# Performance work log

Hardware: AMD Instinct MI355X
Metric: run time of the kernel (lower is better)

## Reference

```python
import jax, jax.numpy as jnp
import numpy as np

N_NODES = 100000
IN_DIM = 64
HID = 128
HID2 = HID // 2
N_CLASSES = 2
N_EDGES = 1600000
BN_EPS = 1e-5


def setup_inputs() -> dict:
    key = jax.random.key(0)
    ks = jax.random.split(key, 12)
    x = jax.random.normal(ks[0], (N_NODES, IN_DIM), dtype=jnp.float32)
    edge_index = jax.random.randint(ks[1], (2, N_EDGES), 0, N_NODES, dtype=jnp.int64)
    s = lambda k, shp, fan: jax.random.normal(k, shp, dtype=jnp.float32) / np.sqrt(fan)
    return {
        "x": x,
        "edge_index": edge_index,
        # SAGEConv1: lin_l (on aggregated neighbors, has bias), lin_r (root, no bias)
        "W1_l": s(ks[2], (IN_DIM, HID), IN_DIM),
        "b1_l": jnp.zeros((HID,), jnp.float32),
        "W1_r": s(ks[3], (IN_DIM, HID), IN_DIM),
        # SAGEConv2
        "W2_l": s(ks[4], (HID, HID2), HID),
        "b2_l": jnp.zeros((HID2,), jnp.float32),
        "W2_r": s(ks[5], (HID, HID2), HID),
        # BatchNorm (eval mode: running stats)
        "bn1_gamma": jnp.ones((HID,), jnp.float32),
        "bn1_beta": jnp.zeros((HID,), jnp.float32),
        "bn1_mean": jax.random.normal(ks[6], (HID,), dtype=jnp.float32) * 0.1,
        "bn1_var": jax.random.uniform(ks[7], (HID,), minval=0.5, maxval=1.5, dtype=jnp.float32),
        "bn2_gamma": jnp.ones((HID2,), jnp.float32),
        "bn2_beta": jnp.zeros((HID2,), jnp.float32),
        "bn2_mean": jax.random.normal(ks[8], (HID2,), dtype=jnp.float32) * 0.1,
        "bn2_var": jax.random.uniform(ks[9], (HID2,), minval=0.5, maxval=1.5, dtype=jnp.float32),
        # classifier
        "Wc": s(ks[10], (HID2, N_CLASSES), HID2),
        "bc": jnp.zeros((N_CLASSES,), jnp.float32),
    }


def _sage_mean(h, src, dst, Wl, bl, Wr, n_nodes):
    # gather source-node features along edges, scatter-mean into destinations
    msg = h[src]                                            # [E, D]
    summed = jax.ops.segment_sum(msg, dst, num_segments=n_nodes)  # [N, D]
    cnt = jax.ops.segment_sum(jnp.ones_like(dst, dtype=h.dtype), dst, num_segments=n_nodes)
    mean = summed / jnp.maximum(cnt, 1.0)[:, None]
    return mean @ Wl + bl + h @ Wr


def _bn_eval(h, gamma, beta, mean, var):
    return (h - mean) * (gamma * jax.lax.rsqrt(var + BN_EPS)) + beta


def reference(x, edge_index, W1_l, b1_l, W1_r, W2_l, b2_l, W2_r,
              bn1_gamma, bn1_beta, bn1_mean, bn1_var,
              bn2_gamma, bn2_beta, bn2_mean, bn2_var, Wc, bc):
    src, dst = edge_index[0], edge_index[1]
    n = x.shape[0]
    h = _sage_mean(x, src, dst, W1_l, b1_l, W1_r, n)
    h = jax.nn.relu(_bn_eval(h, bn1_gamma, bn1_beta, bn1_mean, bn1_var))
    h = _sage_mean(h, src, dst, W2_l, b2_l, W2_r, n)
    h = jax.nn.relu(_bn_eval(h, bn2_gamma, bn2_beta, bn2_mean, bn2_var))
    return h @ Wc + bc  # logits [N, num_classes]
```

## Files before the change

kernel.cpp:

```cpp
#include <hip/hip_runtime.h>
#include <math.h>

#define N_NODES 100000
#define IN_DIM 64
#define HID 128
#define HID2 64
#define N_EDGES 1600000
#define BN_EPS 1e-5f

#define NPB 128
#define NB 782
#define BIN_BLOCKS 391
#define BIN_CHUNK 4096
#define SORT_CAP 4096
#define CAST_BLOCKS 6250

typedef __attribute__((ext_vector_type(8))) __bf16 bf16x8;
typedef __attribute__((ext_vector_type(4))) float f32x4;
typedef __attribute__((ext_vector_type(2))) float f32x2;
typedef __attribute__((ext_vector_type(8))) unsigned short u16x8;

__device__ __forceinline__ unsigned short f2bf(float f) {
    unsigned int u = __builtin_bit_cast(unsigned int, f);
    u += 0x7fffu + ((u >> 16) & 1u);
    return (unsigned short)(u >> 16);
}

__device__ __forceinline__ void accum_fp8x8(float a[8], uint2 v) {
    f32x2 p0 = __builtin_amdgcn_cvt_pk_f32_fp8((int)v.x, false);
    f32x2 p1 = __builtin_amdgcn_cvt_pk_f32_fp8((int)v.x, true);
    f32x2 p2 = __builtin_amdgcn_cvt_pk_f32_fp8((int)v.y, false);
    f32x2 p3 = __builtin_amdgcn_cvt_pk_f32_fp8((int)v.y, true);
    a[0] += p0.x; a[1] += p0.y; a[2] += p1.x; a[3] += p1.y;
    a[4] += p2.x; a[5] += p2.y; a[6] += p3.x; a[7] += p3.y;
}

__global__ __launch_bounds__(256) void prep_all(
    const float* __restrict__ x,
    const float* __restrict__ W1l, const float* __restrict__ W1r,
    const float* __restrict__ W2l, const float* __restrict__ W2r,
    unsigned short* __restrict__ Wf1, unsigned short* __restrict__ Wf2,
    unsigned short* __restrict__ Abuf,
    unsigned char* __restrict__ x8,
    int* __restrict__ bucketTotal)
{
    const int bid = blockIdx.x;
    if (bid < 16) {
        int task = bid * 4 + (threadIdx.x >> 6);
        int lane = threadIdx.x & 63;
        int m  = task >> 5;
        int nt = (task >> 2) & 7;
        int kt = task & 3;
        int col = nt * 16 + (lane & 15);
        int k0  = kt * 32 + (lane >> 4) * 8;
        unsigned short tmp[8];
        #pragma unroll
        for (int e = 0; e < 8; ++e) {
            int k = k0 + e;
            float v;
            if (m == 0) v = (k < 64) ? W1l[k * HID + col] : W1r[(k - 64) * HID + col];
            else        v = (col < 64) ? W2l[k * HID2 + col] : W2r[k * HID2 + (col - 64)];
            tmp[e] = f2bf(v);
        }
        unsigned short* dst = ((m == 0) ? Wf1 : Wf2)
                            + ((size_t)((nt * 4 + kt) * 64 + lane)) * 8;
        *(u16x8*)dst = *(const u16x8*)tmp;
    } else if (bid < 16 + CAST_BLOCKS) {
        int tid = (bid - 16) * 256 + threadIdx.x;
        int node = tid >> 4;
        int q    = tid & 15;
        float4 v = ((const float4*)x)[tid];
        unsigned short o[4] = {f2bf(v.x), f2bf(v.y), f2bf(v.z), f2bf(v.w)};
        *(uint2*)(Abuf + (size_t)node * 128 + 64 + q * 4) = *(const uint2*)o;
        int p = __builtin_amdgcn_cvt_pk_fp8_f32(v.x, v.y, 0, false);
        p     = __builtin_amdgcn_cvt_pk_fp8_f32(v.z, v.w, p, true);
        *(unsigned int*)(x8 + (size_t)node * 64 + q * 4) = (unsigned int)p;
    } else {
        for (int i = threadIdx.x; i < NB; i += 256) bucketTotal[i] = 0;
    }
}

__global__ __launch_bounds__(256) void bin_count(
    const int* __restrict__ dst,
    int* __restrict__ bucketTotal,
    int* __restrict__ perBlockBase)
{
    __shared__ int cnt[NB];
    const int t = threadIdx.x;
    for (int i = t; i < NB; i += 256) cnt[i] = 0;
    __syncthreads();
    const int e40 = blockIdx.x * (BIN_CHUNK / 4);
    const int4* dst4 = (const int4*)dst;
    #pragma unroll
    for (int i = 0; i < BIN_CHUNK / 4 / 256; ++i) {
        int ei = e40 + i * 256 + t;
        if (ei < N_EDGES / 4) {
            int4 d = dst4[ei];
            atomicAdd(&cnt[d.x >> 7], 1);
            atomicAdd(&cnt[d.y >> 7], 1);
            atomicAdd(&cnt[d.z >> 7], 1);
            atomicAdd(&cnt[d.w >> 7], 1);
        }
    }
    __syncthreads();
    for (int b = t; b < NB; b += 256) {
        int c = cnt[b];
        if (c) perBlockBase[blockIdx.x * NB + b] = atomicAdd(&bucketTotal[b], c);
    }
}

__global__ __launch_bounds__(1024) void bucket_scan(
    const int* __restrict__ bucketTotal, int* __restrict__ bucketStart)
{
    __shared__ int s[1024];
    const int t = threadIdx.x;
    int v = (t < NB) ? bucketTotal[t] : 0;
    s[t] = v;
    __syncthreads();
    #pragma unroll
    for (int off = 1; off < 1024; off <<= 1) {
        int u = (t >= off) ? s[t - off] : 0;
        __syncthreads();
        s[t] += u;
        __syncthreads();
    }
    if (t < NB) bucketStart[t] = s[t] - v;
    if (t == 0) bucketStart[NB] = N_EDGES;
}

__global__ __launch_bounds__(256) void bin_write(
    const int* __restrict__ src, const int* __restrict__ dst,
    const int* __restrict__ bucketStart,
    const int* __restrict__ perBlockBase,
    unsigned int* __restrict__ binned)
{
    __shared__ int cur[NB];
    const int t = threadIdx.x;
    for (int i = t; i < NB; i += 256) cur[i] = 0;
    __syncthreads();
    const int e40 = blockIdx.x * (BIN_CHUNK / 4);
    const int4* dst4 = (const int4*)dst;
    const int4* src4 = (const int4*)src;
    #pragma unroll
    for (int i = 0; i < BIN_CHUNK / 4 / 256; ++i) {
        int ei = e40 + i * 256 + t;
        if (ei < N_EDGES / 4) {
            int4 d = dst4[ei];
            int4 s = src4[ei];
            int ds[4] = {d.x, d.y, d.z, d.w};
            int ss[4] = {s.x, s.y, s.z, s.w};
            #pragma unroll
            for (int k = 0; k < 4; ++k) {
                int b = ds[k] >> 7;
                int pos = bucketStart[b] + perBlockBase[blockIdx.x * NB + b]
                        + atomicAdd(&cur[b], 1);
                binned[pos] = ((unsigned int)ss[k] << 7) | (unsigned int)(ds[k] & 127);
            }
        }
    }
}

__global__ __launch_bounds__(256) void bucket_sort(
    const unsigned int* __restrict__ binned,
    const int* __restrict__ bucketStart,
    int* __restrict__ sortedSrc,
    int* __restrict__ rowStart)
{
    __shared__ unsigned int stage[SORT_CAP];
    __shared__ int hist[NPB];
    __shared__ int cur[NPB];

    const int b  = blockIdx.x;
    const int t  = threadIdx.x;
    const int bs = bucketStart[b];
    const int be = bucketStart[b + 1];
    const int total = be - bs;

    if (t < NPB) hist[t] = 0;
    __syncthreads();

    if (total <= SORT_CAP) {
        for (int i = t; i < total; i += 256) {
            unsigned int p = binned[bs + i];
            stage[i] = p;
            atomicAdd(&hist[p & 127], 1);
        }
        __syncthreads();
        int orig = (t < NPB) ? hist[t] : 0;
        __syncthreads();
        #pragma unroll
        for (int off = 1; off < NPB; off <<= 1) {
            int v = (t < NPB && t >= off) ? hist[t - off] : 0;
            __syncthreads();
            if (t < NPB) hist[t] += v;
            __syncthreads();
        }
        if (t < NPB) {
            int excl = hist[t] - orig;
            int node = b * NPB + t;
            if (node < N_NODES) rowStart[node] = bs + excl;
            cur[t] = excl;
        }
        if (b == 0 && t == 0) rowStart[N_NODES] = N_EDGES;
        __syncthreads();
        for (int i = t; i < total; i += 256) {
            unsigned int p = stage[i];
            int pos = atomicAdd(&cur[p & 127], 1);
            sortedSrc[bs + pos] = (int)(p >> 7);
        }
    } else {
        for (int i = t; i < total; i += 256)
            atomicAdd(&hist[binned[bs + i] & 127], 1);
        __syncthreads();
        int orig = (t < NPB) ? hist[t] : 0;
        __syncthreads();
        #pragma unroll
        for (int off = 1; off < NPB; off <<= 1) {
            int v = (t < NPB && t >= off) ? hist[t - off] : 0;
            __syncthreads();
            if (t < NPB) hist[t] += v;
            __syncthreads();
        }
        if (t < NPB) {
            int excl = hist[t] - orig;
            int node = b * NPB + t;
            if (node < N_NODES) rowStart[node] = bs + excl;
            cur[t] = excl;
        }
        if (b == 0 && t == 0) rowStart[N_NODES] = N_EDGES;
        __syncthreads();
        for (int i = t; i < total; i += 256) {
            unsigned int p = binned[bs + i];
            int pos = atomicAdd(&cur[p & 127], 1);
            sortedSrc[bs + pos] = (int)(p >> 7);
        }
    }
}

__global__ __launch_bounds__(256) void gather1_e(
    const int* __restrict__ rowStart,
    const int* __restrict__ sortedSrc,
    const unsigned char* __restrict__ x8,
    unsigned short* __restrict__ Abuf)
{
    const int node = (int)((blockIdx.x * 256u + threadIdx.x) >> 3);
    const int lane = threadIdx.x & 63;
    const int f    = lane & 7;
    const int nb   = lane & 56;
    const int b = rowStart[node], e = rowStart[node + 1];

    float a0[8] = {}, a1[8] = {}, a2[8] = {}, a3[8] = {};

    for (int base = b; base < e; base += 8) {
        const int cnt = min(e - base, 8);
        int srcv = (base + f < e) ? sortedSrc[base + f] : 0;
        int i = 0;
        for (; i + 4 <= cnt; i += 4) {
            int s0 = __shfl(srcv, nb + i);
            int s1 = __shfl(srcv, nb + i + 1);
            int s2 = __shfl(srcv, nb + i + 2);
            int s3 = __shfl(srcv, nb + i + 3);
            accum_fp8x8(a0, *(const uint2*)(x8 + (size_t)s0 * 64 + f * 8));
            accum_fp8x8(a1, *(const uint2*)(x8 + (size_t)s1 * 64 + f * 8));
            accum_fp8x8(a2, *(const uint2*)(x8 + (size_t)s2 * 64 + f * 8));
            accum_fp8x8(a3, *(const uint2*)(x8 + (size_t)s3 * 64 + f * 8));
        }
        for (; i < cnt; ++i) {
            int s0 = __shfl(srcv, nb + i);
            accum_fp8x8(a0, *(const uint2*)(x8 + (size_t)s0 * 64 + f * 8));
        }
    }
    #pragma unroll
    for (int i = 0; i < 8; ++i) a0[i] = (a0[i] + a1[i]) + (a2[i] + a3[i]);

    float inv = 1.0f / fmaxf((float)(e - b), 1.0f);
    unsigned short o[8];
    #pragma unroll
    for (int i = 0; i < 8; ++i) o[i] = f2bf(a0[i] * inv);
    *(uint4*)(Abuf + (size_t)node * 128 + f * 8) = *(const uint4*)o;
}

__global__ __launch_bounds__(256, 4) void gemm_fused_mfma(
    const unsigned short* __restrict__ Abuf,
    const unsigned short* __restrict__ Wf1,
    const unsigned short* __restrict__ Wf2,
    const float* __restrict__ b1l,
    const float* __restrict__ g1, const float* __restrict__ be1,
    const float* __restrict__ m1, const float* __restrict__ v1,
    const float* __restrict__ b2l,
    unsigned char* __restrict__ t1f8,
    unsigned short* __restrict__ r1bf)
{
    __shared__ unsigned short Al[64 * 136];

    const int t = threadIdx.x;
    const int w = t >> 6, l = t & 63;
    const int n0 = blockIdx.x * 64;

    {
        const int node = t >> 2, q = t & 3;
        const int nn = n0 + node;
        const uint4* srcp = (const uint4*)(Abuf + (size_t)nn * 128) + q * 4;
        uint4 z; z.x = z.y = z.z = z.w = 0u;
        unsigned short* drow = &Al[node * 136 + q * 32];
        #pragma unroll
        for (int i = 0; i < 4; ++i) {
            uint4 v = (nn < N_NODES) ? srcp[i] : z;
            *(uint4*)(drow + i * 8) = v;
        }
    }
    __syncthreads();

    const int row = l & 15, kq = l >> 4;

    f32x4 acc[4][2];
    #pragma unroll
    for (int a = 0; a < 4; ++a)
        #pragma unroll
        for (int b = 0; b < 2; ++b) acc[a][b] = (f32x4)(0.0f);

    #pragma unroll
    for (int kt = 0; kt < 4; ++kt) {
        bf16x8 bfr[2];
        #pragma unroll
        for (int n = 0; n < 2; ++n)
            bfr[n] = __builtin_bit_cast(bf16x8,
                *(const u16x8*)(Wf1 + ((size_t)(((2 * w + n) * 4 + kt) * 64 + l)) * 8));
        #pragma unroll
        for (int mt = 0; mt < 4; ++mt) {
            bf16x8 afr = __builtin_bit_cast(bf16x8,
                *(const u16x8*)&Al[(mt * 16 + row) * 136 + kt * 32 + kq * 8]);
            #pragma unroll
            for (int n = 0; n < 2; ++n)
                acc[mt][n] = __builtin_amdgcn_mfma_f32_16x16x32_bf16(
                    afr, bfr[n], acc[mt][n], 0, 0, 0);
        }
    }
    __syncthreads();

    #pragma unroll
    for (int n = 0; n < 2; ++n) {
        int j = w * 32 + n * 16 + (l & 15);
        float s  = g1[j] * rsqrtf(v1[j] + BN_EPS);
        float of = be1[j] + (b1l[j] - m1[j]) * s;
        #pragma unroll
        for (int mt = 0; mt < 4; ++mt) {
            #pragma unroll
            for (int i = 0; i < 4; ++i) {
                float h = fmaxf(fmaf(acc[mt][n][i], s, of), 0.0f);
                Al[(mt * 16 + kq * 4 + i) * 136 + j] = f2bf(h);
            }
        }
    }
    __syncthreads();

    f32x4 acc2[4][2];
    #pragma unroll
    for (int a = 0; a < 4; ++a)
        #pragma unroll
        for (int b = 0; b < 2; ++b) acc2[a][b] = (f32x4)(0.0f);

    #pragma unroll
    for (int kt = 0; kt < 4; ++kt) {
        bf16x8 bfr[2];
        #pragma unroll
        for (int n = 0; n < 2; ++n)
            bfr[n] = __builtin_bit_cast(bf16x8,
                *(const u16x8*)(Wf2 + ((size_t)(((2 * w + n) * 4 + kt) * 64 + l)) * 8));
        #pragma unroll
        for (int mt = 0; mt < 4; ++mt) {
            bf16x8 afr = __builtin_bit_cast(bf16x8,
                *(const u16x8*)&Al[(mt * 16 + row) * 136 + kt * 32 + kq * 8]);
            #pragma unroll
            for (int n = 0; n < 2; ++n)
                acc2[mt][n] = __builtin_amdgcn_mfma_f32_16x16x32_bf16(
                    afr, bfr[n], acc2[mt][n], 0, 0, 0);
        }
    }

    #pragma unroll
    for (int n = 0; n < 2; ++n) {
        int j = w * 32 + n * 16 + (l & 15);
        float bl = (w >= 2) ? b2l[j - 64] : 0.0f;
        #pragma unroll
        for (int mt = 0; mt < 4; ++mt) {
            #pragma unroll
            for (int i = 0; i < 4; ++i) {
                int node = n0 + mt * 16 + kq * 4 + i;
                if (node < N_NODES) {
                    float vv = acc2[mt][n][i];
                    if (w < 2) {
                        int p = __builtin_amdgcn_cvt_pk_fp8_f32(vv, vv, 0, false);
                        t1f8[(size_t)node * 64 + j] = (unsigned char)(p & 0xff);
                    } else {
                        r1bf[(size_t)node * 64 + (j - 64)] = f2bf(vv + bl);
                    }
                }
            }
        }
    }
}

__global__ __launch_bounds__(256) void gather2_e(
    const unsigned char* __restrict__ t1f8,
    const int* __restrict__ rowStart,
    const int* __restrict__ sortedSrc,
    const unsigned short* __restrict__ r1bf,
    const float* __restrict__ g2, const float* __restrict__ be2,
    const float* __restrict__ m2, const float* __restrict__ v2,
    const float* __restrict__ Wc, const float* __restrict__ bc,
    float* __restrict__ out)
{
    const int node = (int)((blockIdx.x * 256u + threadIdx.x) >> 3);
    const int lane = threadIdx.x & 63;
    const int f    = lane & 7;
    const int nb   = lane & 56;
    const int b = rowStart[node], e = rowStart[node + 1];

    float a0[8] = {}, a1[8] = {}, a2[8] = {}, a3[8] = {};

    for (int base = b; base < e; base += 8) {
        const int cnt = min(e - base, 8);
        int srcv = (base + f < e) ? sortedSrc[base + f] : 0;
        int i = 0;
        for (; i + 4 <= cnt; i += 4) {
            int s0 = __shfl(srcv, nb + i);
            int s1 = __shfl(srcv, nb + i + 1);
            int s2 = __shfl(srcv, nb + i + 2);
            int s3 = __shfl(srcv, nb + i + 3);
            accum_fp8x8(a0, *(const uint2*)(t1f8 + (size_t)s0 * 64 + f * 8));
            accum_fp8x8(a1, *(const uint2*)(t1f8 + (size_t)s1 * 64 + f * 8));
            accum_fp8x8(a2, *(const uint2*)(t1f8 + (size_t)s2 * 64 + f * 8));
            accum_fp8x8(a3, *(const uint2*)(t1f8 + (size_t)s3 * 64 + f * 8));
        }
        for (; i < cnt; ++i) {
            int s0 = __shfl(srcv, nb + i);
            accum_fp8x8(a0, *(const uint2*)(t1f8 + (size_t)s0 * 64 + f * 8));
        }
    }
    #pragma unroll
    for (int i = 0; i < 8; ++i) a0[i] = (a0[i] + a1[i]) + (a2[i] + a3[i]);

    const float inv = 1.0f / fmaxf((float)(e - b), 1.0f);
    const int f0 = f * 8;
    uint4 rv = *(const uint4*)(r1bf + (size_t)node * 64 + f0);
    unsigned int rw[4] = {rv.x, rv.y, rv.z, rv.w};
    float l0 = 0.f, l1 = 0.f;
    #pragma unroll
    for (int i = 0; i < 8; ++i) {
        int fe = f0 + i;
        unsigned int w = rw[i >> 1];
        float rr = (i & 1) ? __builtin_bit_cast(float, w)
                           : __builtin_bit_cast(float, w << 16);
        float pre = a0[i] * inv + rr;
        float s   = g2[fe] * rsqrtf(v2[fe] + BN_EPS);
        float h2  = fmaxf((pre - m2[fe]) * s + be2[fe], 0.0f);
        l0 = fmaf(h2, Wc[fe * 2 + 0], l0);
        l1 = fmaf(h2, Wc[fe * 2 + 1], l1);
    }
    #pragma unroll
    for (int off = 4; off > 0; off >>= 1) {
        l0 += __shfl_xor(l0, off);
        l1 += __shfl_xor(l1, off);
    }
    if (f == 0) {
        out[(size_t)node * 2 + 0] = l0 + bc[0];
        out[(size_t)node * 2 + 1] = l1 + bc[1];
    }
}

extern "C" void kernel_launch(void* const* d_in, const int* in_sizes, int n_in,
                              void* d_out, int out_size, void* d_ws, size_t ws_size,
                              hipStream_t stream)
{
    const float* x    = (const float*)d_in[0];
    const int*   eidx = (const int*)d_in[1];
    const float* W1l  = (const float*)d_in[2];
    const float* b1l  = (const float*)d_in[3];
    const float* W1r  = (const float*)d_in[4];
    const float* W2l  = (const float*)d_in[5];
    const float* b2l  = (const float*)d_in[6];
    const float* W2r  = (const float*)d_in[7];
    const float* g1   = (const float*)d_in[8];
    const float* be1  = (const float*)d_in[9];
    const float* m1   = (const float*)d_in[10];
    const float* v1   = (const float*)d_in[11];
    const float* g2   = (const float*)d_in[12];
    const float* be2  = (const float*)d_in[13];
    const float* m2   = (const float*)d_in[14];
    const float* v2   = (const float*)d_in[15];
    const float* Wc   = (const float*)d_in[16];
    const float* bc   = (const float*)d_in[17];
    float* out = (float*)d_out;

    const int* src = eidx;
    const int* dst = eidx + N_EDGES;

    char* ws = (char*)d_ws;
    size_t off = 0;
    auto alloc = [&](size_t bytes) { void* p = ws + off; off = (off + bytes + 255) & ~(size_t)255; return p; };
    int* bucketTotal  = (int*)alloc((size_t)NB * 4);
    int* bucketStart  = (int*)alloc((size_t)(NB + 1) * 4);
    int* perBlockBase = (int*)alloc((size_t)BIN_BLOCKS * NB * 4);
    unsigned int* binned = (unsigned int*)alloc((size_t)N_EDGES * 4);
    int* sortedSrc    = (int*)alloc((size_t)N_EDGES * 4);
    int* rowStart     = (int*)alloc((size_t)(N_NODES + 1) * 4);
    unsigned short* Wf1  = (unsigned short*)alloc(128 * 128 * 2);
    unsigned short* Wf2  = (unsigned short*)alloc(128 * 128 * 2);
    unsigned short* Abuf = (unsigned short*)alloc((size_t)N_NODES * 128 * 2);
    unsigned char*  x8   = (unsigned char*)alloc((size_t)N_NODES * 64);
    unsigned char*  t1f8 = (unsigned char*)alloc((size_t)N_NODES * 64);
    unsigned short* r1bf = (unsigned short*)alloc((size_t)N_NODES * 64 * 2);

    const int gemmGrid    = (N_NODES + 63) / 64;
    const int gatherGrid  = (N_NODES * 8) / 256;

    prep_all<<<16 + CAST_BLOCKS + 1, 256, 0, stream>>>(
        x, W1l, W1r, W2l, W2r, Wf1, Wf2, Abuf, x8, bucketTotal);

    bin_count  <<<BIN_BLOCKS, 256, 0, stream>>>(dst, bucketTotal, perBlockBase);
    bucket_scan<<<1, 1024, 0, stream>>>(bucketTotal, bucketStart);
    bin_write  <<<BIN_BLOCKS, 256, 0, stream>>>(src, dst, bucketStart, perBlockBase, binned);
    bucket_sort<<<NB, 256, 0, stream>>>(binned, bucketStart, sortedSrc, rowStart);

    gather1_e<<<gatherGrid, 256, 0, stream>>>(rowStart, sortedSrc, x8, Abuf);

    gemm_fused_mfma<<<gemmGrid, 256, 0, stream>>>(
        Abuf, Wf1, Wf2, b1l, g1, be1, m1, v1, b2l, t1f8, r1bf);

    gather2_e<<<gatherGrid, 256, 0, stream>>>(
        t1f8, rowStart, sortedSrc, r1bf, g2, be2, m2, v2, Wc, bc, out);
}
```

Before: 139.9 us.

## Fuse layer-1 neighbor gather into the MFMA GEMM kernel via shared memory

Removes the separate gather1 kernel and performs the fp8 neighbor mean aggregation inside the GEMM block, writing results directly into the shared-memory A tile. The Abuf round trip through global memory and one kernel launch are eliminated, and x is now stored as a compact 64-wide bf16 buffer. Each node uses 4 threads loading 16 bytes per edge instead of 8 threads loading 8 bytes. The trade-off is that the GEMM block now carries the irregular gather latency, with fewer threads per node and less memory-level parallelism per node.

```diff
diff --git a/kernel.cpp b/kernel.cpp
--- a/kernel.cpp
+++ b/kernel.cpp
@@ -35,12 +35,23 @@
     a[4] += p2.x; a[5] += p2.y; a[6] += p3.x; a[7] += p3.y;
 }
 
+__device__ __forceinline__ void accum_fp8x16(float a[16], uint4 v) {
+    unsigned int w[4] = {v.x, v.y, v.z, v.w};
+    #pragma unroll
+    for (int k = 0; k < 4; ++k) {
+        f32x2 lo = __builtin_amdgcn_cvt_pk_f32_fp8((int)w[k], false);
+        f32x2 hi = __builtin_amdgcn_cvt_pk_f32_fp8((int)w[k], true);
+        a[4*k+0] += lo.x; a[4*k+1] += lo.y;
+        a[4*k+2] += hi.x; a[4*k+3] += hi.y;
+    }
+}
+
 __global__ __launch_bounds__(256) void prep_all(
     const float* __restrict__ x,
     const float* __restrict__ W1l, const float* __restrict__ W1r,
     const float* __restrict__ W2l, const float* __restrict__ W2r,
     unsigned short* __restrict__ Wf1, unsigned short* __restrict__ Wf2,
-    unsigned short* __restrict__ Abuf,
+    unsigned short* __restrict__ xbf,
     unsigned char* __restrict__ x8,
     int* __restrict__ bucketTotal)
 {
@@ -71,7 +82,7 @@
         int q    = tid & 15;
         float4 v = ((const float4*)x)[tid];
         unsigned short o[4] = {f2bf(v.x), f2bf(v.y), f2bf(v.z), f2bf(v.w)};
-        *(uint2*)(Abuf + (size_t)node * 128 + 64 + q * 4) = *(const uint2*)o;
+        *(uint2*)(xbf + (size_t)node * 64 + q * 4) = *(const uint2*)o;
         int p = __builtin_amdgcn_cvt_pk_fp8_f32(v.x, v.y, 0, false);
         p     = __builtin_amdgcn_cvt_pk_fp8_f32(v.z, v.w, p, true);
         *(unsigned int*)(x8 + (size_t)node * 64 + q * 4) = (unsigned int)p;
@@ -237,51 +248,11 @@
     }
 }
 
-__global__ __launch_bounds__(256) void gather1_e(
+__global__ __launch_bounds__(256, 4) void gemm_fused_g(
     const int* __restrict__ rowStart,
     const int* __restrict__ sortedSrc,
     const unsigned char* __restrict__ x8,
-    unsigned short* __restrict__ Abuf)
-{
-    const int node = (int)((blockIdx.x * 256u + threadIdx.x) >> 3);
-    const int lane = threadIdx.x & 63;
-    const int f    = lane & 7;
-    const int nb   = lane & 56;
-    const int b = rowStart[node], e = rowStart[node + 1];
-
-    float a0[8] = {}, a1[8] = {}, a2[8] = {}, a3[8] = {};
-
-    for (int base = b; base < e; base += 8) {
-        const int cnt = min(e - base, 8);
-        int srcv = (base + f < e) ? sortedSrc[base + f] : 0;
-        int i = 0;
-        for (; i + 4 <= cnt; i += 4) {
-            int s0 = __shfl(srcv, nb + i);
-            int s1 = __shfl(srcv, nb + i + 1);
-            int s2 = __shfl(srcv, nb + i + 2);
-            int s3 = __shfl(srcv, nb + i + 3);
-            accum_fp8x8(a0, *(const uint2*)(x8 + (size_t)s0 * 64 + f * 8));
-            accum_fp8x8(a1, *(const uint2*)(x8 + (size_t)s1 * 64 + f * 8));
-            accum_fp8x8(a2, *(const uint2*)(x8 + (size_t)s2 * 64 + f * 8));
-            accum_fp8x8(a3, *(const uint2*)(x8 + (size_t)s3 * 64 + f * 8));
-        }
-        for (; i < cnt; ++i) {
-            int s0 = __shfl(srcv, nb + i);
-            accum_fp8x8(a0, *(const uint2*)(x8 + (size_t)s0 * 64 + f * 8));
-        }
-    }
-    #pragma unroll
-    for (int i = 0; i < 8; ++i) a0[i] = (a0[i] + a1[i]) + (a2[i] + a3[i]);
-
-    float inv = 1.0f / fmaxf((float)(e - b), 1.0f);
-    unsigned short o[8];
-    #pragma unroll
-    for (int i = 0; i < 8; ++i) o[i] = f2bf(a0[i] * inv);
-    *(uint4*)(Abuf + (size_t)node * 128 + f * 8) = *(const uint4*)o;
-}
-
-__global__ __launch_bounds__(256, 4) void gemm_fused_mfma(
-    const unsigned short* __restrict__ Abuf,
+    const unsigned short* __restrict__ xbf,
     const unsigned short* __restrict__ Wf1,
     const unsigned short* __restrict__ Wf2,
     const float* __restrict__ b1l,
@@ -296,17 +267,64 @@
     const int t = threadIdx.x;
     const int w = t >> 6, l = t & 63;
     const int n0 = blockIdx.x * 64;
+    const int r   = t >> 2;
+    const int sub = t & 3;
+    const int gb  = l & 60;
+    const int node = n0 + r;
 
     {
-        const int node = t >> 2, q = t & 3;
-        const int nn = n0 + node;
-        const uint4* srcp = (const uint4*)(Abuf + (size_t)nn * 128) + q * 4;
-        uint4 z; z.x = z.y = z.z = z.w = 0u;
-        unsigned short* drow = &Al[node * 136 + q * 32];
-        #pragma unroll
-        for (int i = 0; i < 4; ++i) {
-            uint4 v = (nn < N_NODES) ? srcp[i] : z;
-            *(uint4*)(drow + i * 8) = v;
+        unsigned short* drow = &Al[r * 136 + 64 + sub * 16];
+        if (node < N_NODES) {
+            const uint4* sp = (const uint4*)(xbf + (size_t)node * 64 + sub * 16);
+            uint4 v0 = sp[0], v1 = sp[1];
+            *(uint4*)drow = v0;
+            *(uint4*)(drow + 8) = v1;
+        } else {
+            uint4 z; z.x = z.y = z.z = z.w = 0u;
+            *(uint4*)drow = z;
+            *(uint4*)(drow + 8) = z;
+        }
+    }
+
+    {
+        unsigned short* drow = &Al[r * 136 + sub * 16];
+        if (node < N_NODES) {
+            const int b = rowStart[node], e = rowStart[node + 1];
+            float a[16] = {};
+            for (int base = b; base < e; base += 4) {
+                const int cnt = min(e - base, 4);
+                int srcv = (base + sub < e) ? sortedSrc[base + sub] : 0;
+                if (cnt == 4) {
+                    int s0 = __shfl(srcv, gb + 0);
+                    int s1 = __shfl(srcv, gb + 1);
+                    int s2 = __shfl(srcv, gb + 2);
+                    int s3 = __shfl(srcv, gb + 3);
+                    uint4 v0 = *(const uint4*)(x8 + (size_t)s0 * 64 + sub * 16);
+                    uint4 v1 = *(const uint4*)(x8 + (size_t)s1 * 64 + sub * 16);
+                    uint4 v2 = *(const uint4*)(x8 + (size_t)s2 * 64 + sub * 16);
+                    uint4 v3 = *(const uint4*)(x8 + (size_t)s3 * 64 + sub * 16);
+                    accum_fp8x16(a, v0);
+                    accum_fp8x16(a, v1);
+                    accum_fp8x16(a, v2);
+                    accum_fp8x16(a, v3);
+                } else {
+                    for (int i = 0; i < cnt; ++i) {
+                        int s0 = __shfl(srcv, gb + i);
+                        uint4 v0 = *(const uint4*)(x8 + (size_t)s0 * 64 + sub * 16);
+                        accum_fp8x16(a, v0);
+                    }
+                }
+            }
+            float inv = 1.0f / fmaxf((float)(e - b), 1.0f);
+            unsigned short o[16];
+            #pragma unroll
+            for (int i = 0; i < 16; ++i) o[i] = f2bf(a[i] * inv);
+            *(uint4*)drow       = *(const uint4*)o;
+            *(uint4*)(drow + 8) = *(const uint4*)(o + 8);
+        } else {
+            uint4 z; z.x = z.y = z.z = z.w = 0u;
+            *(uint4*)drow = z;
+            *(uint4*)(drow + 8) = z;
         }
     }
     __syncthreads();
@@ -386,14 +404,14 @@
         for (int mt = 0; mt < 4; ++mt) {
             #pragma unroll
             for (int i = 0; i < 4; ++i) {
-                int node = n0 + mt * 16 + kq * 4 + i;
-                if (node < N_NODES) {
+                int nn = n0 + mt * 16 + kq * 4 + i;
+                if (nn < N_NODES) {
                     float vv = acc2[mt][n][i];
                     if (w < 2) {
                         int p = __builtin_amdgcn_cvt_pk_fp8_f32(vv, vv, 0, false);
-                        t1f8[(size_t)node * 64 + j] = (unsigned char)(p & 0xff);
+                        t1f8[(size_t)nn * 64 + j] = (unsigned char)(p & 0xff);
                     } else {
-                        r1bf[(size_t)node * 64 + (j - 64)] = f2bf(vv + bl);
+                        r1bf[(size_t)nn * 64 + (j - 64)] = f2bf(vv + bl);
                     }
                 }
             }
@@ -449,9 +467,9 @@
     #pragma unroll
     for (int i = 0; i < 8; ++i) {
         int fe = f0 + i;
-        unsigned int w = rw[i >> 1];
-        float rr = (i & 1) ? __builtin_bit_cast(float, w)
-                           : __builtin_bit_cast(float, w << 16);
+        unsigned int wv = rw[i >> 1];
+        float rr = (i & 1) ? __builtin_bit_cast(float, wv)
+                           : __builtin_bit_cast(float, wv << 16);
         float pre = a0[i] * inv + rr;
         float s   = g2[fe] * rsqrtf(v2[fe] + BN_EPS);
         float h2  = fmaxf((pre - m2[fe]) * s + be2[fe], 0.0f);
@@ -507,7 +525,7 @@
     int* rowStart     = (int*)alloc((size_t)(N_NODES + 1) * 4);
     unsigned short* Wf1  = (unsigned short*)alloc(128 * 128 * 2);
     unsigned short* Wf2  = (unsigned short*)alloc(128 * 128 * 2);
-    unsigned short* Abuf = (unsigned short*)alloc((size_t)N_NODES * 128 * 2);
+    unsigned short* xbf  = (unsigned short*)alloc((size_t)N_NODES * 64 * 2);
     unsigned char*  x8   = (unsigned char*)alloc((size_t)N_NODES * 64);
     unsigned char*  t1f8 = (unsigned char*)alloc((size_t)N_NODES * 64);
     unsigned short* r1bf = (unsigned short*)alloc((size_t)N_NODES * 64 * 2);
@@ -516,17 +534,16 @@
     const int gatherGrid  = (N_NODES * 8) / 256;
 
     prep_all<<<16 + CAST_BLOCKS + 1, 256, 0, stream>>>(
-        x, W1l, W1r, W2l, W2r, Wf1, Wf2, Abuf, x8, bucketTotal);
+        x, W1l, W1r, W2l, W2r, Wf1, Wf2, xbf, x8, bucketTotal);
 
     bin_count  <<<BIN_BLOCKS, 256, 0, stream>>>(dst, bucketTotal, perBlockBase);
     bucket_scan<<<1, 1024, 0, stream>>>(bucketTotal, bucketStart);
     bin_write  <<<BIN_BLOCKS, 256, 0, stream>>>(src, dst, bucketStart, perBlockBase, binned);
     bucket_sort<<<NB, 256, 0, stream>>>(binned, bucketStart, sortedSrc, rowStart);
 
-    gather1_e<<<gatherGrid, 256, 0, stream>>>(rowStart, sortedSrc, x8, Abuf);
-
-    gemm_fused_mfma<<<gemmGrid, 256, 0, stream>>>(
-        Abuf, Wf1, Wf2, b1l, g1, be1, m1, v1, b2l, t1f8, r1bf);
+    gemm_fused_g<<<gemmGrid, 256, 0, stream>>>(
+        rowStart, sortedSrc, x8, xbf, Wf1, Wf2,
+        b1l, g1, be1, m1, v1, b2l, t1f8, r1bf);
 
     gather2_e<<<gatherGrid, 256, 0, stream>>>(
         t1f8, rowStart, sortedSrc, r1bf, g2, be2, m2, v2, Wc, bc, out);
```

New measurement: 135.6 us. -3.1%, faster.
